# Performance work log

Hardware: AMD Instinct MI355X
Metric: run time of the kernel (lower is better)

## Reference

```python
import jax, jax.numpy as jnp
import numpy as np

NUM_GROUPS = 16
EPS = 1e-05
VARIANCE_FLOOR = 1e-06


def setup_inputs() -> dict:
    key = jax.random.key(0)
    k1, k2, k3, k4 = jax.random.split(key, 4)
    B, L, D, G = 4, 4096, 2048, NUM_GROUPS
    return {
        "x": jax.random.normal(k1, (B, L, D), dtype=jnp.float32),
        "prev_count": jnp.zeros((B,), dtype=jnp.int64 if jax.config.jax_enable_x64 else jnp.int32),
        "prev_mean": jax.random.normal(k2, (B, G), dtype=jnp.float32),
        "prev_var": jnp.ones((B, G), dtype=jnp.float32),
        "padding_mask": jnp.ones((B, L), dtype=bool),
        "weight": 0.1 * jax.random.normal(k3, (D,), dtype=jnp.float32),
        "bias": 0.1 * jax.random.normal(k4, (D,), dtype=jnp.float32),
    }


def reference(x, prev_count, prev_mean, prev_var, padding_mask, weight, bias):
    B, L, D = x.shape
    G = NUM_GROUPS
    gs = D // G
    x_groups = x.reshape(B, L, G, gs)                      # (B,L,G,gs)
    valid = padding_mask.astype(x.dtype)                   # (B,L)
    valid_exp = valid[..., None]                           # (B,L,1)

    group_means = x_groups.mean(axis=-1)                   # (B,L,G)
    prev_count_f = prev_count.astype(x.dtype)              # (B,)
    prev_sum = prev_mean * prev_count_f[:, None]           # (B,G)

    # streaming (cumsum-based Welford) mean
    cumsum_means = jnp.cumsum(group_means * valid_exp, axis=1)
    sum_t = prev_sum[:, None, :] + cumsum_means            # (B,L,G)
    count_t = prev_count_f[:, None] + jnp.cumsum(valid, axis=1)  # (B,L)
    count_clamped = jnp.maximum(count_t, 1.0)
    mean_t = jnp.where(count_t[..., None] > 0.0,
                       sum_t / count_clamped[..., None],
                       prev_mean[:, None, :])               # (B,L,G)

    # Welford M2 accumulation via prefix sums
    mean_prev = jnp.concatenate([prev_mean[:, None, :], mean_t[:, :-1, :]], axis=1)
    delta = group_means - mean_prev
    delta2 = group_means - mean_t
    prev_m2 = prev_var * jnp.maximum(prev_count_f, 1.0)[:, None]  # (B,G)
    m2_t = prev_m2[:, None, :] + jnp.cumsum(delta * delta2 * valid_exp, axis=1)
    var_t = jnp.where(count_t[..., None] > 0.0,
                      m2_t / count_clamped[..., None],
                      prev_var[:, None, :])
    var_t = jnp.maximum(var_t, VARIANCE_FLOOR)

    # normalize + affine
    x_hat = (x_groups - mean_t[..., None]) * jax.lax.rsqrt(var_t[..., None] + EPS)
    scale = (weight + 1.0).reshape(1, 1, G, gs)
    shift = bias.reshape(1, 1, G, gs)
    y = (x_hat * scale + shift).reshape(B, L, D)

    new_count = prev_count + padding_mask.astype(prev_count.dtype).sum(axis=1)
    return y, new_count, mean_t[:, -1, :], var_t[:, -1, :]
```

## Files before the change

kernel.cpp:

```cpp
#include <hip/hip_runtime.h>

#define NGROUPS 16
#define TPG     16
#define CHUNK   8
#define EPS_F   1e-5f
#define VFLOOR  1e-6f

typedef float v4f __attribute__((ext_vector_type(4)));

__device__ __forceinline__ float sum8(const float4& a, const float4& b) {
    return ((a.x + a.y) + (a.z + a.w)) + ((b.x + b.y) + (b.z + b.w));
}

__device__ __forceinline__ void wmerge(float& na, float& ma, float& m2a,
                                       float nb, float mb, float m2b) {
    if (nb > 0.f) {
        float nn = na + nb;
        float d  = mb - ma;
        float r  = nb / nn;
        ma  = fmaf(d, r, ma);
        m2a = m2a + m2b + d * d * (na * r);
        na  = nn;
    }
}

__global__ void __launch_bounds__(256)
ts_gm_agg(const float* __restrict__ x, const int* __restrict__ mask,
          float* __restrict__ gm_buf, float4* __restrict__ loc4,
          int B, int L, int D, int NC, float inv_gs)
{
    const int b   = blockIdx.x / NC;
    const int c   = blockIdx.x % NC;
    const int tid = threadIdx.x;
    const int g   = tid / TPG;
    const bool leader = (tid & (TPG - 1)) == 0;
    const int t0  = c * CHUNK;
    const int t1  = min(t0 + CHUNK, L);

    const float* xb = x + (size_t)b * L * D + tid * 8;
    const int*   mb = mask + (size_t)b * L;
    float* gmo = gm_buf + (((size_t)b * NC + c) * NGROUPS + g) * CHUNK;

    float n = 0.f, mean = 0.f, m2 = 0.f;
    #pragma unroll
    for (int t = t0; t < t1; ++t) {
        const float4* p = (const float4*)(xb + (size_t)t * D);
        float4 v0 = p[0], v1 = p[1];
        float s = sum8(v0, v1);
        s += __shfl_xor(s, 1, 64);
        s += __shfl_xor(s, 2, 64);
        s += __shfl_xor(s, 4, 64);
        s += __shfl_xor(s, 8, 64);
        float gmv = s * inv_gs;
        if (leader) gmo[t - t0] = gmv;
        if (mb[t]) {
            n += 1.f;
            float d = gmv - mean;
            mean += __fdividef(d, n);
            m2 = fmaf(d, gmv - mean, m2);
        }
    }
    if (leader) {
        loc4[((size_t)b * NGROUPS + g) * NC + c] = make_float4(n, mean, m2, 0.f);
    }
}

__global__ void __launch_bounds__(256)
ts_fused(const float* __restrict__ x, const int* __restrict__ mask,
         const float* __restrict__ gm_buf, const float4* __restrict__ loc4,
         const int* __restrict__ prev_count, const float* __restrict__ prev_mean,
         const float* __restrict__ prev_var,
         const float* __restrict__ weight, const float* __restrict__ bias,
         float* __restrict__ y, float* __restrict__ out_count,
         float* __restrict__ out_mean, float* __restrict__ out_var,
         int B, int L, int D, int NC)
{
    __shared__ float s_mean[NGROUPS][CHUNK + 1];
    __shared__ float s_rstd[NGROUPS][CHUNK + 1];

    const int b   = blockIdx.x / NC;
    const int c   = blockIdx.x % NC;
    const int tid = threadIdx.x;
    const int g   = tid / TPG;
    const int k   = tid & (TPG - 1);
    const int chain = b * NGROUPS + g;

    float n = 0.f, mean = 0.f, m2 = 0.f;
    const float4* lrow = loc4 + (size_t)chain * NC;
    for (int cp = k; cp < c; cp += TPG) {
        float4 v = lrow[cp];
        wmerge(n, mean, m2, v.x, v.y, v.z);
    }
    #pragma unroll
    for (int o = 1; o < TPG; o <<= 1) {
        float on = __shfl_xor(n, o, 64);
        float om = __shfl_xor(mean, o, 64);
        float o2 = __shfl_xor(m2, o, 64);
        wmerge(n, mean, m2, on, om, o2);
    }
    {
        float pn = (float)prev_count[b];
        float pm = prev_mean[chain];
        float p2 = prev_var[chain] * fmaxf(pn, 1.0f);
        wmerge(pn, pm, p2, n, mean, m2);
        n = pn; mean = pm; m2 = p2;
    }

    const int t0 = c * CHUNK;
    const int jmax = min(CHUNK, L - t0);
    if (k == 0) {
        const float* gmo = gm_buf + (((size_t)b * NC + c) * NGROUPS + g) * CHUNK;
        const int*   mrow = mask + (size_t)b * L + t0;
        float var = fmaxf(__fdividef(m2, fmaxf(n, 1.f)), VFLOOR);
        #pragma unroll
        for (int j = 0; j < jmax; ++j) {
            float gmv = gmo[j];
            if (mrow[j]) {
                n += 1.f;
                float d = gmv - mean;
                mean += __fdividef(d, n);
                m2 = fmaf(d, gmv - mean, m2);
            }
            var = fmaxf(__fdividef(m2, fmaxf(n, 1.f)), VFLOOR);
            s_mean[g][j] = mean;
            s_rstd[g][j] = rsqrtf(var + EPS_F);
        }
        if (c == NC - 1) {
            out_mean[chain] = mean;
            out_var[chain]  = var;
            if (g == 0) out_count[b] = n;
        }
    }

    const float4* wp = (const float4*)(weight + tid * 8);
    const float4* hp = (const float4*)(bias + tid * 8);
    float4 w0 = wp[0], w1 = wp[1];
    float4 h0 = hp[0], h1 = hp[1];
    w0.x += 1.f; w0.y += 1.f; w0.z += 1.f; w0.w += 1.f;
    w1.x += 1.f; w1.y += 1.f; w1.z += 1.f; w1.w += 1.f;

    __syncthreads();

    const float* xb = x + ((size_t)b * L + t0) * D + tid * 8;
    float*       yb = y + ((size_t)b * L + t0) * D + tid * 8;
    #pragma unroll 2
    for (int j = 0; j < jmax; ++j) {
        float m_ = s_mean[g][j];
        float r_ = s_rstd[g][j];
        const float4* p = (const float4*)(xb + (size_t)j * D);
        float4 v0 = p[0], v1 = p[1];
        v4f o0, o1;
        o0.x = fmaf((v0.x - m_) * r_, w0.x, h0.x);
        o0.y = fmaf((v0.y - m_) * r_, w0.y, h0.y);
        o0.z = fmaf((v0.z - m_) * r_, w0.z, h0.z);
        o0.w = fmaf((v0.w - m_) * r_, w0.w, h0.w);
        o1.x = fmaf((v1.x - m_) * r_, w1.x, h1.x);
        o1.y = fmaf((v1.y - m_) * r_, w1.y, h1.y);
        o1.z = fmaf((v1.z - m_) * r_, w1.z, h1.z);
        o1.w = fmaf((v1.w - m_) * r_, w1.w, h1.w);
        v4f* q = (v4f*)(yb + (size_t)j * D);
        __builtin_nontemporal_store(o0, q);
        __builtin_nontemporal_store(o1, q + 1);
    }
}

extern "C" void kernel_launch(void* const* d_in, const int* in_sizes, int n_in,
                              void* d_out, int out_size, void* d_ws, size_t ws_size,
                              hipStream_t stream) {
    const float* x          = (const float*)d_in[0];
    const int*   prev_count = (const int*)d_in[1];
    const float* prev_mean  = (const float*)d_in[2];
    const float* prev_var   = (const float*)d_in[3];
    const int*   mask       = (const int*)d_in[4];
    const float* weight     = (const float*)d_in[5];
    const float* bias       = (const float*)d_in[6];

    const int B  = in_sizes[1];
    const int D  = in_sizes[5];
    const int L  = in_sizes[4] / B;
    const int NC = (L + CHUNK - 1) / CHUNK;
    const int BG = B * NGROUPS;
    const float inv_gs = (float)NGROUPS / (float)D;

    float* out = (float*)d_out;
    const size_t yN = (size_t)B * L * D;
    float* out_y     = out;
    float* out_count = out + yN;
    float* out_mean  = out + yN + B;
    float* out_var   = out + yN + B + BG;

    float* ws = (float*)d_ws;
    const size_t gmN = (size_t)B * NC * NGROUPS * CHUNK;
    float*  gm_buf = ws;
    float4* loc4   = (float4*)(ws + gmN);

    dim3 blk(D / 8);

    ts_gm_agg<<<B * NC, blk, 0, stream>>>(x, mask, gm_buf, loc4, B, L, D, NC, inv_gs);

    ts_fused<<<B * NC, blk, 0, stream>>>(x, mask, gm_buf, loc4,
                                         prev_count, prev_mean, prev_var,
                                         weight, bias,
                                         out_y, out_count, out_mean, out_var,
                                         B, L, D, NC);
}
```

Baseline: 275.2 us.

## Split into group-mean, dedicated scan, and normalize kernels

Replaces the two-kernel design, where every normalize block re-merged all preceding chunk aggregates (a quadratic cost over chunks), with three kernels. The first writes group means per chain. A scan kernel runs one block per (batch, group) chain and does a parallel Welford prefix merge in shared memory, writing a per-timestep mean and rstd. A simple normalize kernel then reads those values. This removes the redundant prefix merges at the cost of an extra launch and an extra small intermediate buffer.

```diff
diff --git a/kernel.cpp b/kernel.cpp
--- a/kernel.cpp
+++ b/kernel.cpp
@@ -25,9 +25,8 @@
 }
 
 __global__ void __launch_bounds__(256)
-ts_gm_agg(const float* __restrict__ x, const int* __restrict__ mask,
-          float* __restrict__ gm_buf, float4* __restrict__ loc4,
-          int B, int L, int D, int NC, float inv_gs)
+k_gm(const float* __restrict__ x, float* __restrict__ gm,
+     int B, int L, int D, int NC, float inv_gs)
 {
     const int b   = blockIdx.x / NC;
     const int c   = blockIdx.x % NC;
@@ -38,10 +37,8 @@
     const int t1  = min(t0 + CHUNK, L);
 
     const float* xb = x + (size_t)b * L * D + tid * 8;
-    const int*   mb = mask + (size_t)b * L;
-    float* gmo = gm_buf + (((size_t)b * NC + c) * NGROUPS + g) * CHUNK;
-
-    float n = 0.f, mean = 0.f, m2 = 0.f;
+    float* gmr = gm + ((size_t)b * NGROUPS + g) * L;
+
     #pragma unroll
     for (int t = t0; t < t1; ++t) {
         const float4* p = (const float4*)(xb + (size_t)t * D);
@@ -51,86 +48,95 @@
         s += __shfl_xor(s, 2, 64);
         s += __shfl_xor(s, 4, 64);
         s += __shfl_xor(s, 8, 64);
-        float gmv = s * inv_gs;
-        if (leader) gmo[t - t0] = gmv;
-        if (mb[t]) {
+        if (leader) gmr[t] = s * inv_gs;
+    }
+}
+
+__global__ void __launch_bounds__(256)
+k_scan(const float* __restrict__ gm, const int* __restrict__ mask,
+       const int* __restrict__ prev_count, const float* __restrict__ prev_mean,
+       const float* __restrict__ prev_var,
+       float2* __restrict__ ms, float* __restrict__ out_count,
+       float* __restrict__ out_mean, float* __restrict__ out_var,
+       int B, int L)
+{
+    __shared__ float sn[256], sm[256], s2[256];
+
+    const int chain = blockIdx.x;
+    const int b   = chain / NGROUPS;
+    const int g   = chain - b * NGROUPS;
+    const int tid = threadIdx.x;
+    const int TPT = (L + 255) / 256;
+    const int t0  = tid * TPT;
+    const int t1  = min(t0 + TPT, L);
+
+    const float* gmr = gm + (size_t)chain * L;
+    const int*   mr  = mask + (size_t)b * L;
+
+    float n = 0.f, m = 0.f, m2 = 0.f;
+    for (int t = t0; t < t1; ++t) {
+        if (mr[t]) {
             n += 1.f;
-            float d = gmv - mean;
-            mean += __fdividef(d, n);
-            m2 = fmaf(d, gmv - mean, m2);
+            float gmv = gmr[t];
+            float d = gmv - m;
+            m += __fdividef(d, n);
+            m2 = fmaf(d, gmv - m, m2);
         }
     }
-    if (leader) {
-        loc4[((size_t)b * NGROUPS + g) * NC + c] = make_float4(n, mean, m2, 0.f);
+
+    float cn = n, cm = m, c2 = m2;
+    sn[tid] = cn; sm[tid] = cm; s2[tid] = c2;
+    __syncthreads();
+    #pragma unroll
+    for (int o = 1; o < 256; o <<= 1) {
+        float tn = 0.f, tm = 0.f, t2 = 0.f;
+        const bool h = (tid >= o);
+        if (h) { tn = sn[tid - o]; tm = sm[tid - o]; t2 = s2[tid - o]; }
+        __syncthreads();
+        if (h) { wmerge(tn, tm, t2, cn, cm, c2); cn = tn; cm = tm; c2 = t2; }
+        sn[tid] = cn; sm[tid] = cm; s2[tid] = c2;
+        __syncthreads();
+    }
+
+    float en = 0.f, em = 0.f, e2 = 0.f;
+    if (tid > 0) { en = sn[tid - 1]; em = sm[tid - 1]; e2 = s2[tid - 1]; }
+    float pn = (float)prev_count[b];
+    float pm = prev_mean[chain];
+    float p2 = prev_var[chain] * fmaxf(pn, 1.0f);
+    wmerge(pn, pm, p2, en, em, e2);
+
+    float2* msr = ms + (size_t)chain * L;
+    float rn = pn, rm = pm, r2 = p2;
+    float var = fmaxf(__fdividef(r2, fmaxf(rn, 1.f)), VFLOOR);
+    for (int t = t0; t < t1; ++t) {
+        float gmv = gmr[t];
+        if (mr[t]) {
+            rn += 1.f;
+            float d = gmv - rm;
+            rm += __fdividef(d, rn);
+            r2 = fmaf(d, gmv - rm, r2);
+        }
+        var = fmaxf(__fdividef(r2, fmaxf(rn, 1.f)), VFLOOR);
+        msr[t] = make_float2(rm, rsqrtf(var + EPS_F));
+    }
+    if (t0 <= L - 1 && L - 1 < t1) {
+        out_mean[chain] = rm;
+        out_var[chain]  = var;
+        if (g == 0) out_count[b] = rn;
     }
 }
 
 __global__ void __launch_bounds__(256)
-ts_fused(const float* __restrict__ x, const int* __restrict__ mask,
-         const float* __restrict__ gm_buf, const float4* __restrict__ loc4,
-         const int* __restrict__ prev_count, const float* __restrict__ prev_mean,
-         const float* __restrict__ prev_var,
-         const float* __restrict__ weight, const float* __restrict__ bias,
-         float* __restrict__ y, float* __restrict__ out_count,
-         float* __restrict__ out_mean, float* __restrict__ out_var,
-         int B, int L, int D, int NC)
+k_norm(const float* __restrict__ x, const float2* __restrict__ ms,
+       const float* __restrict__ weight, const float* __restrict__ bias,
+       float* __restrict__ y, int B, int L, int D, int NC)
 {
-    __shared__ float s_mean[NGROUPS][CHUNK + 1];
-    __shared__ float s_rstd[NGROUPS][CHUNK + 1];
-
     const int b   = blockIdx.x / NC;
     const int c   = blockIdx.x % NC;
     const int tid = threadIdx.x;
     const int g   = tid / TPG;
-    const int k   = tid & (TPG - 1);
-    const int chain = b * NGROUPS + g;
-
-    float n = 0.f, mean = 0.f, m2 = 0.f;
-    const float4* lrow = loc4 + (size_t)chain * NC;
-    for (int cp = k; cp < c; cp += TPG) {
-        float4 v = lrow[cp];
-        wmerge(n, mean, m2, v.x, v.y, v.z);
-    }
-    #pragma unroll
-    for (int o = 1; o < TPG; o <<= 1) {
-        float on = __shfl_xor(n, o, 64);
-        float om = __shfl_xor(mean, o, 64);
-        float o2 = __shfl_xor(m2, o, 64);
-        wmerge(n, mean, m2, on, om, o2);
-    }
-    {
-        float pn = (float)prev_count[b];
-        float pm = prev_mean[chain];
-        float p2 = prev_var[chain] * fmaxf(pn, 1.0f);
-        wmerge(pn, pm, p2, n, mean, m2);
-        n = pn; mean = pm; m2 = p2;
-    }
-
-    const int t0 = c * CHUNK;
+    const int t0  = c * CHUNK;
     const int jmax = min(CHUNK, L - t0);
-    if (k == 0) {
-        const float* gmo = gm_buf + (((size_t)b * NC + c) * NGROUPS + g) * CHUNK;
-        const int*   mrow = mask + (size_t)b * L + t0;
-        float var = fmaxf(__fdividef(m2, fmaxf(n, 1.f)), VFLOOR);
-        #pragma unroll
-        for (int j = 0; j < jmax; ++j) {
-            float gmv = gmo[j];
-            if (mrow[j]) {
-                n += 1.f;
-                float d = gmv - mean;
-                mean += __fdividef(d, n);
-                m2 = fmaf(d, gmv - mean, m2);
-            }
-            var = fmaxf(__fdividef(m2, fmaxf(n, 1.f)), VFLOOR);
-            s_mean[g][j] = mean;
-            s_rstd[g][j] = rsqrtf(var + EPS_F);
-        }
-        if (c == NC - 1) {
-            out_mean[chain] = mean;
-            out_var[chain]  = var;
-            if (g == 0) out_count[b] = n;
-        }
-    }
 
     const float4* wp = (const float4*)(weight + tid * 8);
     const float4* hp = (const float4*)(bias + tid * 8);
@@ -139,28 +145,35 @@
     w0.x += 1.f; w0.y += 1.f; w0.z += 1.f; w0.w += 1.f;
     w1.x += 1.f; w1.y += 1.f; w1.z += 1.f; w1.w += 1.f;
 
-    __syncthreads();
-
-    const float* xb = x + ((size_t)b * L + t0) * D + tid * 8;
-    float*       yb = y + ((size_t)b * L + t0) * D + tid * 8;
-    #pragma unroll 2
-    for (int j = 0; j < jmax; ++j) {
-        float m_ = s_mean[g][j];
-        float r_ = s_rstd[g][j];
-        const float4* p = (const float4*)(xb + (size_t)j * D);
-        float4 v0 = p[0], v1 = p[1];
-        v4f o0, o1;
-        o0.x = fmaf((v0.x - m_) * r_, w0.x, h0.x);
-        o0.y = fmaf((v0.y - m_) * r_, w0.y, h0.y);
-        o0.z = fmaf((v0.z - m_) * r_, w0.z, h0.z);
-        o0.w = fmaf((v0.w - m_) * r_, w0.w, h0.w);
-        o1.x = fmaf((v1.x - m_) * r_, w1.x, h1.x);
-        o1.y = fmaf((v1.y - m_) * r_, w1.y, h1.y);
-        o1.z = fmaf((v1.z - m_) * r_, w1.z, h1.z);
-        o1.w = fmaf((v1.w - m_) * r_, w1.w, h1.w);
-        v4f* q = (v4f*)(yb + (size_t)j * D);
-        __builtin_nontemporal_store(o0, q);
-        __builtin_nontemporal_store(o1, q + 1);
+    const float2* msr = ms + ((size_t)b * NGROUPS + g) * L + t0;
+    const float*  xb  = x + ((size_t)b * L + t0) * D + tid * 8;
+    float*        yb  = y + ((size_t)b * L + t0) * D + tid * 8;
+
+    float2 st[CHUNK];
+    #pragma unroll
+    for (int j = 0; j < CHUNK; ++j)
+        if (j < jmax) st[j] = msr[j];
+
+    #pragma unroll
+    for (int j = 0; j < CHUNK; ++j) {
+        if (j < jmax) {
+            const float m_ = st[j].x;
+            const float r_ = st[j].y;
+            const float4* p = (const float4*)(xb + (size_t)j * D);
+            float4 v0 = p[0], v1 = p[1];
+            v4f o0, o1;
+            o0.x = fmaf((v0.x - m_) * r_, w0.x, h0.x);
+            o0.y = fmaf((v0.y - m_) * r_, w0.y, h0.y);
+            o0.z = fmaf((v0.z - m_) * r_, w0.z, h0.z);
+            o0.w = fmaf((v0.w - m_) * r_, w0.w, h0.w);
+            o1.x = fmaf((v1.x - m_) * r_, w1.x, h1.x);
+            o1.y = fmaf((v1.y - m_) * r_, w1.y, h1.y);
+            o1.z = fmaf((v1.z - m_) * r_, w1.z, h1.z);
+            o1.w = fmaf((v1.w - m_) * r_, w1.w, h1.w);
+            v4f* q = (v4f*)(yb + (size_t)j * D);
+            __builtin_nontemporal_store(o0, q);
+            __builtin_nontemporal_store(o1, q + 1);
+        }
     }
 }
 
@@ -189,18 +202,16 @@
     float* out_mean  = out + yN + B;
     float* out_var   = out + yN + B + BG;
 
-    float* ws = (float*)d_ws;
-    const size_t gmN = (size_t)B * NC * NGROUPS * CHUNK;
-    float*  gm_buf = ws;
-    float4* loc4   = (float4*)(ws + gmN);
+    float* gm = (float*)d_ws;
+    const size_t gmN = (size_t)BG * L;
+    float2* ms = (float2*)(gm + gmN);
 
     dim3 blk(D / 8);
 
-    ts_gm_agg<<<B * NC, blk, 0, stream>>>(x, mask, gm_buf, loc4, B, L, D, NC, inv_gs);
-
-    ts_fused<<<B * NC, blk, 0, stream>>>(x, mask, gm_buf, loc4,
-                                         prev_count, prev_mean, prev_var,
-                                         weight, bias,
-                                         out_y, out_count, out_mean, out_var,
-                                         B, L, D, NC);
-}
+    k_gm  <<<B * NC, blk, 0, stream>>>(x, gm, B, L, D, NC, inv_gs);
+
+    k_scan<<<BG, 256, 0, stream>>>(gm, mask, prev_count, prev_mean, prev_var,
+                                   ms, out_count, out_mean, out_var, B, L);
+
+    k_norm<<<B * NC, blk, 0, stream>>>(x, ms, weight, bias, out_y, B, L, D, NC);
+}
```

Result: slower. 288.1 us (+4.7%).
